# Kernel optimization log

Hardware: AMD Instinct MI355X
Metric: run time of the kernel (lower is better)

## Reference

```python
import jax, jax.numpy as jnp
import numpy as np

NUM_TAGS = 64
START_TAG = 62
STOP_TAG = 63
NEG = -10000.0
B, L = 512, 512


def setup_inputs() -> dict:
    key = jax.random.key(0)
    k1, k2, k3 = jax.random.split(key, 3)
    inputs = jax.random.normal(k1, (B, L, NUM_TAGS), dtype=jnp.float32)
    tags = jax.random.randint(k2, (B, L), 0, 62)  # real tags only (exclude sentinels)
    mask = jnp.ones((B, L), dtype=jnp.int32)
    transitions = jax.random.normal(k3, (NUM_TAGS, NUM_TAGS), dtype=jnp.float32)
    # match torch __init__: transitions[start_tag, :] = -10000; transitions[:, stop_tag] = -10000
    transitions = transitions.at[START_TAG, :].set(NEG).at[:, STOP_TAG].set(NEG)
    return {"inputs": inputs, "tags": tags, "mask": mask, "transitions": transitions}


def crf_loss(inputs, transitions, tags, mask):
    # inputs: [B, L, T] emissions; transitions[next, prev]; tags/mask: [B, L]
    Bb, Ll, T = inputs.shape
    maskf = mask.astype(inputs.dtype)

    # ---- denominator: forward algorithm (log-sum-exp recurrence over time) ----
    init_alphas = jnp.full((Bb, T), NEG, dtype=inputs.dtype).at[:, START_TAG].set(0.0)

    def step(forward_var, xs):
        emit, m = xs  # emit: [B, T], m: [B]
        # scores[b, next, prev] = fv[b, prev] + (transitions[next, prev] + emit[b, next]) * m[b]
        scores = forward_var[:, None, :] + (transitions[None, :, :] + emit[:, :, None]) * m[:, None, None]
        return jax.nn.logsumexp(scores, axis=-1), None

    forward_var, _ = jax.lax.scan(step, init_alphas, (jnp.swapaxes(inputs, 0, 1), maskf.T))
    terminal = forward_var + transitions[STOP_TAG][None, :]
    log_denominator = jax.nn.logsumexp(terminal, axis=-1)  # [B]

    # ---- numerator: score of the gold tag sequence (fully vectorized over time) ----
    score = transitions[tags[:, 0], START_TAG]  # [B]
    prev_t, next_t = tags[:, :-1], tags[:, 1:]
    trans_sc = transitions[next_t, prev_t]  # [B, L-1]
    emit_sc = jnp.take_along_axis(inputs[:, :-1, :], prev_t[:, :, None], axis=2)[..., 0]  # [B, L-1]
    score = score + jnp.sum(trans_sc * maskf[:, 1:] + emit_sc * maskf[:, :-1], axis=1)
    last_emit = jnp.take_along_axis(inputs[:, -1, :], tags[:, -1:], axis=1)[:, 0]
    score = score + transitions[STOP_TAG, tags[:, -1]] + last_emit * maskf[:, -1]

    return jnp.sum(score - log_denominator)


def reference(inputs, tags, mask, transitions):
    return crf_loss(inputs, transitions, tags, mask)
```

## Files before the change

### kernel.cpp

```cpp
#include <hip/hip_runtime.h>

namespace {

typedef float v2f __attribute__((ext_vector_type(2)));

constexpr int NTAGS = 64;
constexpr int START_T = 62;
constexpr int STOP_T = 63;
constexpr int Bc = 512;
constexpr int Lc = 512;

template <int CTRL>
__device__ __forceinline__ float dpp_add(float x) {
  return x + __int_as_float(__builtin_amdgcn_update_dpp(
                 0, __float_as_int(x), CTRL, 0xf, 0xf, true));
}

__device__ __forceinline__ float wave_max(float v) {
#pragma unroll
  for (int off = 32; off >= 1; off >>= 1)
    v = fmaxf(v, __shfl_xor(v, off, 64));
  return v;
}

__device__ __forceinline__ float wave_sum(float v) {
#pragma unroll
  for (int off = 32; off >= 1; off >>= 1)
    v += __shfl_xor(v, off, 64);
  return v;
}

__global__ __launch_bounds__(64, 1) void crf_scan(
    const float* __restrict__ inputs,
    const int* __restrict__ tags,
    const int* __restrict__ mask,
    const float* __restrict__ trans,
    float* __restrict__ partial) {
  __shared__ float4 vb4[16];
  float* vb1 = reinterpret_cast<float*>(vb4);

  const int b = blockIdx.x;
  const int lane = threadIdx.x;
  const int lr = lane >> 2;
  const int c = lane & 3;

#define DECLE(k) v2f E##k##_0, E##k##_1, E##k##_2, E##k##_3, \
                     E##k##_4, E##k##_5, E##k##_6, E##k##_7;
  DECLE(0) DECLE(1) DECLE(2) DECLE(3)
#define LOADE(k)                                                       \
  {                                                                    \
    const float* tp = trans + (lr + 16 * k) * NTAGS + 4 * c;           \
    E##k##_0 = (v2f){__expf(tp[0]),  __expf(tp[16])};                  \
    E##k##_1 = (v2f){__expf(tp[32]), __expf(tp[48])};                  \
    E##k##_2 = (v2f){__expf(tp[1]),  __expf(tp[17])};                  \
    E##k##_3 = (v2f){__expf(tp[33]), __expf(tp[49])};                  \
    E##k##_4 = (v2f){__expf(tp[2]),  __expf(tp[18])};                  \
    E##k##_5 = (v2f){__expf(tp[34]), __expf(tp[50])};                  \
    E##k##_6 = (v2f){__expf(tp[3]),  __expf(tp[19])};                  \
    E##k##_7 = (v2f){__expf(tp[35]), __expf(tp[51])};                  \
  }
  LOADE(0) LOADE(1) LOADE(2) LOADE(3)

  const float* emit_base = inputs + (size_t)b * Lc * NTAGS;
  const int* mask_b = mask + b * Lc;
  const int* tags_b = tags + b * Lc;

  int Msum = 0;
  vb1[lane] = (lane == 59) ? 1.0f : 0.0f;
  __builtin_amdgcn_wave_barrier();

#define ROWF(k)                                                        \
    v2f a##k##0 = E##k##_0 * (v2f){u0.x, u0.y};                        \
    v2f a##k##1 = E##k##_1 * (v2f){u0.z, u0.w};                        \
    a##k##0 += E##k##_2 * (v2f){u1.x, u1.y};                           \
    a##k##1 += E##k##_3 * (v2f){u1.z, u1.w};                           \
    a##k##0 += E##k##_4 * (v2f){u2.x, u2.y};                           \
    a##k##1 += E##k##_5 * (v2f){u2.z, u2.w};                           \
    a##k##0 += E##k##_6 * (v2f){u3.x, u3.y};                           \
    a##k##1 += E##k##_7 * (v2f){u3.z, u3.w};

#define STEP(W0, W1, W2, W3, MIDX)                                     \
  {                                                                    \
    float4 u0 = vb4[4 * c + 0], u1 = vb4[4 * c + 1];                   \
    float4 u2 = vb4[4 * c + 2], u3 = vb4[4 * c + 3];                   \
        \
    const int sb = __builtin_amdgcn_readlane(__float_as_int(u0.x), 0); \
    const unsigned e0 = ((unsigned)sb >> 23) & 0xffu;                  \
    const int d = (e0 == 0u) ? 0 : (int)e0 - 127;                      \
    Msum += d;                                                         \
    const float rs = __uint_as_float((unsigned)(127 - d) << 23);       \
    const int mv = __builtin_amdgcn_readlane(mrow, (MIDX));            \
    float s0, s1, s2, s3;                                              \
    if (mv) {                                                          \
      ROWF(0) ROWF(1) ROWF(2) ROWF(3)                                  \
      v2f t0 = a00 + a01, t1 = a10 + a11;                              \
      v2f t2 = a20 + a21, t3 = a30 + a31;                              \
      s0 = t0.x + t0.y; s1 = t1.x + t1.y;                              \
      s2 = t2.x + t2.y; s3 = t3.x + t3.y;                              \
      s0 = dpp_add<0xB1>(s0); s1 = dpp_add<0xB1>(s1);                  \
      s2 = dpp_add<0xB1>(s2); s3 = dpp_add<0xB1>(s3);                  \
      s0 = dpp_add<0x4E>(s0); s1 = dpp_add<0x4E>(s1);                  \
      s2 = dpp_add<0x4E>(s2); s3 = dpp_add<0x4E>(s3);                  \
      s0 *= (W0) * rs; s1 *= (W1) * rs;                                \
      s2 *= (W2) * rs; s3 *= (W3) * rs;                                \
    } else {                                                           \
      v2f q0 = ((v2f){u0.x, u0.y} + (v2f){u0.z, u0.w}) +               \
               ((v2f){u1.x, u1.y} + (v2f){u1.z, u1.w});                \
      v2f q1 = ((v2f){u2.x, u2.y} + (v2f){u2.z, u2.w}) +               \
               ((v2f){u3.x, u3.y} + (v2f){u3.z, u3.w});                \
      v2f q = q0 + q1;                                                 \
      float ss = q.x + q.y;                                            \
      ss = dpp_add<0xB1>(ss); ss = dpp_add<0x4E>(ss);                  \
      ss *= rs;                                                        \
      s0 = s1 = s2 = s3 = ss;                                          \
    }                                                                  \
    __builtin_amdgcn_wave_barrier();                                   \
    if ((lane & 3) == 0) vb4[lr] = make_float4(s0, s1, s2, s3);        \
    __builtin_amdgcn_wave_barrier();                                   \
  }

  float wA[4][4], wB[4][4];
#define PRE(Wb, ST)                                                    \
  {                                                                    \
    int s_ = (ST); s_ = s_ > (Lc - 4) ? (Lc - 4) : s_;                 \
    _Pragma("unroll") for (int q = 0; q < 4; ++q) {                    \
      const float* pp = emit_base + (size_t)(s_ + q) * NTAGS + lr;     \
      Wb[q][0] = __expf(pp[0]);                                        \
      Wb[q][1] = __expf(pp[16]);                                       \
      Wb[q][2] = __expf(pp[32]);                                       \
      Wb[q][3] = __expf(pp[48]);                                       \
    }                                                                  \
  }

  PRE(wA, 0)
  int mrow = mask_b[lane];

  for (int chunk = 0; chunk < 8; ++chunk) {
    const int cbase = chunk * 64;
    int mrow_nxt = mask_b[(chunk < 7 ? cbase + 64 : cbase) + lane];
    for (int gp = 0; gp < 8; ++gp) {
      const int base = cbase + gp * 8;
      const int mb = gp * 8;
      PRE(wB, base + 4)
      STEP(wA[0][0], wA[0][1], wA[0][2], wA[0][3], mb + 0)
      STEP(wA[1][0], wA[1][1], wA[1][2], wA[1][3], mb + 1)
      STEP(wA[2][0], wA[2][1], wA[2][2], wA[2][3], mb + 2)
      STEP(wA[3][0], wA[3][1], wA[3][2], wA[3][3], mb + 3)
      PRE(wA, base + 8)
      STEP(wB[0][0], wB[0][1], wB[0][2], wB[0][3], mb + 4)
      STEP(wB[1][0], wB[1][1], wB[1][2], wB[1][3], mb + 5)
      STEP(wB[2][0], wB[2][1], wB[2][2], wB[2][3], mb + 6)
      STEP(wB[3][0], wB[3][1], wB[3][2], wB[3][3], mb + 7)
    }
    mrow = mrow_nxt;
  }

  const float mf = (float)Msum;
  const float C = fmaf(mf, -2.1219444e-4f, mf * 0.693359375f);

  const int sig = ((lane & 15) << 2) | (lane >> 4);
  float alphav = __logf(vb1[sig]) + C;
  float term = alphav + trans[STOP_T * NTAGS + lane];
  float mx = wave_max(term);
  float sden = wave_sum(__expf(term - mx));
  float logden = mx + __logf(sden);

  float sc = 0.0f;
  for (int l = lane; l < Lc; l += 64) {
    int tl = tags_b[l];
    float mfl = (float)mask_b[l];
    if (l < Lc - 1) {
      int tn = tags_b[l + 1];
      float mfn = (float)mask_b[l + 1];
      sc += trans[tn * NTAGS + tl] * mfn +
            emit_base[(size_t)l * NTAGS + tl] * mfl;
    } else {
      sc += trans[STOP_T * NTAGS + tl] +
            emit_base[(size_t)l * NTAGS + tl] * mfl;
    }
  }
  if (lane == 0) sc += trans[tags_b[0] * NTAGS + START_T];
  float score = wave_sum(sc);

  if (lane == 0) partial[b] = score - logden;
}

__global__ void crf_reduce(const float* __restrict__ partial,
                           float* __restrict__ out) {
  const int lane = threadIdx.x;
  float s = 0.0f;
  for (int i = lane; i < Bc; i += 64) s += partial[i];
  s = wave_sum(s);
  if (lane == 0) out[0] = s;
}

}

extern "C" void kernel_launch(void* const* d_in, const int* in_sizes, int n_in,
                              void* d_out, int out_size, void* d_ws,
                              size_t ws_size, hipStream_t stream) {
  const float* inputs = (const float*)d_in[0];
  const int* tags = (const int*)d_in[1];
  const int* mask = (const int*)d_in[2];
  const float* trans = (const float*)d_in[3];
  float* out = (float*)d_out;
  float* partial = (float*)d_ws;

  crf_scan<<<Bc, 64, 0, stream>>>(inputs, tags, mask, trans, partial);
  crf_reduce<<<1, 64, 0, stream>>>(partial, out);
}
```

Baseline: 157.9 us.

## Interleave four batch chains per wave and split numerator into separate kernel

Each wave now runs the forward recurrence for four sequences at once, interleaving their independent steps to hide LDS and DPP latency in the serial chain. The numerator score moves into its own kernel, and the reduce combines the two. Each step also loads its next state vector right after the LDS write, and every lane writes one element instead of quad-leader float4 stores. In exchange there are only 128 blocks on a 256-CU part, so fewer CUs are busy, and register pressure rises from the four sets of prefetched emission weights.

```diff
diff --git a/kernel.cpp b/kernel.cpp
--- a/kernel.cpp
+++ b/kernel.cpp
@@ -9,6 +9,7 @@
 constexpr int STOP_T = 63;
 constexpr int Bc = 512;
 constexpr int Lc = 512;
+constexpr int NCH = 4;
 
 template <int CTRL>
 __device__ __forceinline__ float dpp_add(float x) {
@@ -32,17 +33,15 @@
 
 __global__ __launch_bounds__(64, 1) void crf_scan(
     const float* __restrict__ inputs,
-    const int* __restrict__ tags,
     const int* __restrict__ mask,
     const float* __restrict__ trans,
-    float* __restrict__ partial) {
-  __shared__ float4 vb4[16];
-  float* vb1 = reinterpret_cast<float*>(vb4);
-
-  const int b = blockIdx.x;
+    float* __restrict__ den) {
+  __shared__ float4 vb4[NCH][16];
+
   const int lane = threadIdx.x;
   const int lr = lane >> 2;
   const int c = lane & 3;
+  const int bbase = blockIdx.x * NCH;
 
 #define DECLE(k) v2f E##k##_0, E##k##_1, E##k##_2, E##k##_3, \
                      E##k##_4, E##k##_5, E##k##_6, E##k##_7;
@@ -61,109 +60,156 @@
   }
   LOADE(0) LOADE(1) LOADE(2) LOADE(3)
 
-  const float* emit_base = inputs + (size_t)b * Lc * NTAGS;
-  const int* mask_b = mask + b * Lc;
-  const int* tags_b = tags + b * Lc;
-
-  int Msum = 0;
-  vb1[lane] = (lane == 59) ? 1.0f : 0.0f;
+#define DECLC(i)                                                       \
+  float4 u0_##i, u1_##i, u2_##i, u3_##i;                               \
+  float wA_##i[4][4], wB_##i[4][4];                                    \
+  int Ms_##i = 0, mr_##i, mrn_##i;                                     \
+  const float* pe_##i = inputs + (size_t)(bbase + i) * Lc * NTAGS + lr;\
+  const int* mp_##i = mask + (size_t)(bbase + i) * Lc;
+  DECLC(0) DECLC(1) DECLC(2) DECLC(3)
+
+#pragma unroll
+  for (int i = 0; i < NCH; ++i)
+    ((float*)&vb4[i][0])[lane] = (lane == 59) ? 1.0f : 0.0f;
   __builtin_amdgcn_wave_barrier();
 
-#define ROWF(k)                                                        \
-    v2f a##k##0 = E##k##_0 * (v2f){u0.x, u0.y};                        \
-    v2f a##k##1 = E##k##_1 * (v2f){u0.z, u0.w};                        \
-    a##k##0 += E##k##_2 * (v2f){u1.x, u1.y};                           \
-    a##k##1 += E##k##_3 * (v2f){u1.z, u1.w};                           \
-    a##k##0 += E##k##_4 * (v2f){u2.x, u2.y};                           \
-    a##k##1 += E##k##_5 * (v2f){u2.z, u2.w};                           \
-    a##k##0 += E##k##_6 * (v2f){u3.x, u3.y};                           \
-    a##k##1 += E##k##_7 * (v2f){u3.z, u3.w};
-
-#define STEP(W0, W1, W2, W3, MIDX)                                     \
-  {                                                                    \
-    float4 u0 = vb4[4 * c + 0], u1 = vb4[4 * c + 1];                   \
-    float4 u2 = vb4[4 * c + 2], u3 = vb4[4 * c + 3];                   \
-        \
-    const int sb = __builtin_amdgcn_readlane(__float_as_int(u0.x), 0); \
+#define ULOAD(i)                                                       \
+  {                                                                    \
+    u0_##i = vb4[i][4 * c + 0];                                        \
+    u1_##i = vb4[i][4 * c + 1];                                        \
+    u2_##i = vb4[i][4 * c + 2];                                        \
+    u3_##i = vb4[i][4 * c + 3];                                        \
+  }
+  ULOAD(0) ULOAD(1) ULOAD(2) ULOAD(3)
+
+#define ROWF(k, i)                                                     \
+    v2f a##k##0 = E##k##_0 * (v2f){u0_##i.x, u0_##i.y};                \
+    v2f a##k##1 = E##k##_1 * (v2f){u0_##i.z, u0_##i.w};                \
+    a##k##0 += E##k##_2 * (v2f){u1_##i.x, u1_##i.y};                   \
+    a##k##1 += E##k##_3 * (v2f){u1_##i.z, u1_##i.w};                   \
+    a##k##0 += E##k##_4 * (v2f){u2_##i.x, u2_##i.y};                   \
+    a##k##1 += E##k##_5 * (v2f){u2_##i.z, u2_##i.w};                   \
+    a##k##0 += E##k##_6 * (v2f){u3_##i.x, u3_##i.y};                   \
+    a##k##1 += E##k##_7 * (v2f){u3_##i.z, u3_##i.w};
+
+#define STEP(i, W0, W1, W2, W3, MIDX)                                  \
+  {                                                                    \
+    const int sb =                                                     \
+        __builtin_amdgcn_readfirstlane(__float_as_int(u0_##i.x));      \
     const unsigned e0 = ((unsigned)sb >> 23) & 0xffu;                  \
     const int d = (e0 == 0u) ? 0 : (int)e0 - 127;                      \
-    Msum += d;                                                         \
+    Ms_##i += d;                                                       \
     const float rs = __uint_as_float((unsigned)(127 - d) << 23);       \
-    const int mv = __builtin_amdgcn_readlane(mrow, (MIDX));            \
+    const int mv = __builtin_amdgcn_readlane(mr_##i, (MIDX));          \
     float s0, s1, s2, s3;                                              \
-    if (mv) {                                                          \
-      ROWF(0) ROWF(1) ROWF(2) ROWF(3)                                  \
+    if (__builtin_expect(mv, 1)) {                                     \
+      ROWF(0, i) ROWF(1, i) ROWF(2, i) ROWF(3, i)                      \
       v2f t0 = a00 + a01, t1 = a10 + a11;                              \
       v2f t2 = a20 + a21, t3 = a30 + a31;                              \
-      s0 = t0.x + t0.y; s1 = t1.x + t1.y;                              \
-      s2 = t2.x + t2.y; s3 = t3.x + t3.y;                              \
-      s0 = dpp_add<0xB1>(s0); s1 = dpp_add<0xB1>(s1);                  \
-      s2 = dpp_add<0xB1>(s2); s3 = dpp_add<0xB1>(s3);                  \
-      s0 = dpp_add<0x4E>(s0); s1 = dpp_add<0x4E>(s1);                  \
-      s2 = dpp_add<0x4E>(s2); s3 = dpp_add<0x4E>(s3);                  \
-      s0 *= (W0) * rs; s1 *= (W1) * rs;                                \
-      s2 *= (W2) * rs; s3 *= (W3) * rs;                                \
+      float r0 = t0.x + t0.y, r1 = t1.x + t1.y;                        \
+      float r2 = t2.x + t2.y, r3 = t3.x + t3.y;                        \
+      r0 = dpp_add<0xB1>(r0); r1 = dpp_add<0xB1>(r1);                  \
+      r2 = dpp_add<0xB1>(r2); r3 = dpp_add<0xB1>(r3);                  \
+      r0 = dpp_add<0x4E>(r0); r1 = dpp_add<0x4E>(r1);                  \
+      r2 = dpp_add<0x4E>(r2); r3 = dpp_add<0x4E>(r3);                  \
+      s0 = r0 * ((W0) * rs); s1 = r1 * ((W1) * rs);                    \
+      s2 = r2 * ((W2) * rs); s3 = r3 * ((W3) * rs);                    \
     } else {                                                           \
-      v2f q0 = ((v2f){u0.x, u0.y} + (v2f){u0.z, u0.w}) +               \
-               ((v2f){u1.x, u1.y} + (v2f){u1.z, u1.w});                \
-      v2f q1 = ((v2f){u2.x, u2.y} + (v2f){u2.z, u2.w}) +               \
-               ((v2f){u3.x, u3.y} + (v2f){u3.z, u3.w});                \
-      v2f q = q0 + q1;                                                 \
-      float ss = q.x + q.y;                                            \
+      v2f q0 = ((v2f){u0_##i.x, u0_##i.y} + (v2f){u0_##i.z, u0_##i.w}) + \
+               ((v2f){u1_##i.x, u1_##i.y} + (v2f){u1_##i.z, u1_##i.w}); \
+      v2f q1 = ((v2f){u2_##i.x, u2_##i.y} + (v2f){u2_##i.z, u2_##i.w}) + \
+               ((v2f){u3_##i.x, u3_##i.y} + (v2f){u3_##i.z, u3_##i.w}); \
+      v2f qq = q0 + q1;                                                \
+      float ss = qq.x + qq.y;                                          \
       ss = dpp_add<0xB1>(ss); ss = dpp_add<0x4E>(ss);                  \
       ss *= rs;                                                        \
       s0 = s1 = s2 = s3 = ss;                                          \
     }                                                                  \
+        \
+    const float slo = (c & 1) ? s1 : s0;                               \
+    const float shi = (c & 1) ? s3 : s2;                               \
+    const float sw = (c & 2) ? shi : slo;                              \
     __builtin_amdgcn_wave_barrier();                                   \
-    if ((lane & 3) == 0) vb4[lr] = make_float4(s0, s1, s2, s3);        \
+    ((float*)&vb4[i][0])[lane] = sw;                                   \
     __builtin_amdgcn_wave_barrier();                                   \
-  }
-
-  float wA[4][4], wB[4][4];
-#define PRE(Wb, ST)                                                    \
+    ULOAD(i)                                                           \
+  }
+
+#define PRE(W, i, ST)                                                  \
   {                                                                    \
     int s_ = (ST); s_ = s_ > (Lc - 4) ? (Lc - 4) : s_;                 \
-    _Pragma("unroll") for (int q = 0; q < 4; ++q) {                    \
-      const float* pp = emit_base + (size_t)(s_ + q) * NTAGS + lr;     \
-      Wb[q][0] = __expf(pp[0]);                                        \
-      Wb[q][1] = __expf(pp[16]);                                       \
-      Wb[q][2] = __expf(pp[32]);                                       \
-      Wb[q][3] = __expf(pp[48]);                                       \
+    _Pragma("unroll") for (int q_ = 0; q_ < 4; ++q_) {                 \
+      const float* pp = pe_##i + (size_t)(s_ + q_) * NTAGS;            \
+      W[q_][0] = __expf(pp[0]);                                        \
+      W[q_][1] = __expf(pp[16]);                                       \
+      W[q_][2] = __expf(pp[32]);                                       \
+      W[q_][3] = __expf(pp[48]);                                       \
     }                                                                  \
   }
 
-  PRE(wA, 0)
-  int mrow = mask_b[lane];
+  PRE(wA_0, 0, 0) PRE(wA_1, 1, 0) PRE(wA_2, 2, 0) PRE(wA_3, 3, 0)
+  mr_0 = mp_0[lane]; mr_1 = mp_1[lane];
+  mr_2 = mp_2[lane]; mr_3 = mp_3[lane];
+
+#define S4(BANK, S, MIDX)                                              \
+  STEP(0, BANK##_0[S][0], BANK##_0[S][1], BANK##_0[S][2],              \
+       BANK##_0[S][3], MIDX)                                           \
+  STEP(1, BANK##_1[S][0], BANK##_1[S][1], BANK##_1[S][2],              \
+       BANK##_1[S][3], MIDX)                                           \
+  STEP(2, BANK##_2[S][0], BANK##_2[S][1], BANK##_2[S][2],              \
+       BANK##_2[S][3], MIDX)                                           \
+  STEP(3, BANK##_3[S][0], BANK##_3[S][1], BANK##_3[S][2],              \
+       BANK##_3[S][3], MIDX)
 
   for (int chunk = 0; chunk < 8; ++chunk) {
     const int cbase = chunk * 64;
-    int mrow_nxt = mask_b[(chunk < 7 ? cbase + 64 : cbase) + lane];
+    const int nb = (chunk < 7 ? cbase + 64 : cbase) + lane;
+    mrn_0 = mp_0[nb]; mrn_1 = mp_1[nb];
+    mrn_2 = mp_2[nb]; mrn_3 = mp_3[nb];
     for (int gp = 0; gp < 8; ++gp) {
       const int base = cbase + gp * 8;
       const int mb = gp * 8;
-      PRE(wB, base + 4)
-      STEP(wA[0][0], wA[0][1], wA[0][2], wA[0][3], mb + 0)
-      STEP(wA[1][0], wA[1][1], wA[1][2], wA[1][3], mb + 1)
-      STEP(wA[2][0], wA[2][1], wA[2][2], wA[2][3], mb + 2)
-      STEP(wA[3][0], wA[3][1], wA[3][2], wA[3][3], mb + 3)
-      PRE(wA, base + 8)
-      STEP(wB[0][0], wB[0][1], wB[0][2], wB[0][3], mb + 4)
-      STEP(wB[1][0], wB[1][1], wB[1][2], wB[1][3], mb + 5)
-      STEP(wB[2][0], wB[2][1], wB[2][2], wB[2][3], mb + 6)
-      STEP(wB[3][0], wB[3][1], wB[3][2], wB[3][3], mb + 7)
+      PRE(wB_0, 0, base + 4) PRE(wB_1, 1, base + 4)
+      PRE(wB_2, 2, base + 4) PRE(wB_3, 3, base + 4)
+      S4(wA, 0, mb + 0)
+      S4(wA, 1, mb + 1)
+      S4(wA, 2, mb + 2)
+      S4(wA, 3, mb + 3)
+      PRE(wA_0, 0, base + 8) PRE(wA_1, 1, base + 8)
+      PRE(wA_2, 2, base + 8) PRE(wA_3, 3, base + 8)
+      S4(wB, 0, mb + 4)
+      S4(wB, 1, mb + 5)
+      S4(wB, 2, mb + 6)
+      S4(wB, 3, mb + 7)
     }
-    mrow = mrow_nxt;
-  }
-
-  const float mf = (float)Msum;
-  const float C = fmaf(mf, -2.1219444e-4f, mf * 0.693359375f);
+    mr_0 = mrn_0; mr_1 = mrn_1; mr_2 = mrn_2; mr_3 = mrn_3;
+  }
 
   const int sig = ((lane & 15) << 2) | (lane >> 4);
-  float alphav = __logf(vb1[sig]) + C;
-  float term = alphav + trans[STOP_T * NTAGS + lane];
-  float mx = wave_max(term);
-  float sden = wave_sum(__expf(term - mx));
-  float logden = mx + __logf(sden);
+  const float* tstop = trans + STOP_T * NTAGS;
+#define EPI(i)                                                         \
+  {                                                                    \
+    const float mf_ = (float)Ms_##i;                                   \
+    const float C_ = fmaf(mf_, -2.1219444e-4f, mf_ * 0.693359375f);    \
+    float alphav = __logf(((const float*)&vb4[i][0])[sig]) + C_;       \
+    float term = alphav + tstop[lane];                                 \
+    float mx = wave_max(term);                                         \
+    float sden = wave_sum(__expf(term - mx));                          \
+    if (lane == 0) den[bbase + i] = mx + __logf(sden);                 \
+  }
+  EPI(0) EPI(1) EPI(2) EPI(3)
+}
+
+__global__ void crf_num(const float* __restrict__ inputs,
+                        const int* __restrict__ tags,
+                        const int* __restrict__ mask,
+                        const float* __restrict__ trans,
+                        float* __restrict__ num) {
+  const int b = blockIdx.x;
+  const int lane = threadIdx.x;
+  const float* emit_base = inputs + (size_t)b * Lc * NTAGS;
+  const int* tags_b = tags + b * Lc;
+  const int* mask_b = mask + b * Lc;
 
   float sc = 0.0f;
   for (int l = lane; l < Lc; l += 64) {
@@ -181,15 +227,15 @@
   }
   if (lane == 0) sc += trans[tags_b[0] * NTAGS + START_T];
   float score = wave_sum(sc);
-
-  if (lane == 0) partial[b] = score - logden;
-}
-
-__global__ void crf_reduce(const float* __restrict__ partial,
+  if (lane == 0) num[b] = score;
+}
+
+__global__ void crf_reduce(const float* __restrict__ num,
+                           const float* __restrict__ den,
                            float* __restrict__ out) {
   const int lane = threadIdx.x;
   float s = 0.0f;
-  for (int i = lane; i < Bc; i += 64) s += partial[i];
+  for (int i = lane; i < Bc; i += 64) s += num[i] - den[i];
   s = wave_sum(s);
   if (lane == 0) out[0] = s;
 }
@@ -204,8 +250,10 @@
   const int* mask = (const int*)d_in[2];
   const float* trans = (const float*)d_in[3];
   float* out = (float*)d_out;
-  float* partial = (float*)d_ws;
-
-  crf_scan<<<Bc, 64, 0, stream>>>(inputs, tags, mask, trans, partial);
-  crf_reduce<<<1, 64, 0, stream>>>(partial, out);
-}
+  float* num = (float*)d_ws;
+  float* den = num + Bc;
+
+  crf_scan<<<Bc / NCH, 64, 0, stream>>>(inputs, mask, trans, den);
+  crf_num<<<Bc, 64, 0, stream>>>(inputs, tags, mask, trans, num);
+  crf_reduce<<<1, 64, 0, stream>>>(num, den, out);
+}
```

New measurement: 478.5 us. +203.1%, slower.

## Split CRF forward recurrence into forward and backward halves meeting at midpoint

Applied to the files above, without the earlier changes.

The serial 512-step log-space recurrence is split into a forward pass over the first 256 steps and a backward pass over the last 256 steps, each run by its own workgroup (2*B blocks). The halves are joined by a dot product in a new join kernel, so the serial dependency chain per block is halved and twice as many waves are launched to fill the GPU. The numerator moves to its own kernel, and the scale exponent is now tracked via readfirstlane of the value being written instead of re-reading LDS. This adds two kernel launches and a workspace round trip, and it changes how rescaling and masked steps are handled in the backward direction.

```diff
diff --git a/kernel.cpp b/kernel.cpp
--- a/kernel.cpp
+++ b/kernel.cpp
@@ -9,18 +9,12 @@
 constexpr int STOP_T = 63;
 constexpr int Bc = 512;
 constexpr int Lc = 512;
+constexpr int HL = 256;
 
 template <int CTRL>
 __device__ __forceinline__ float dpp_add(float x) {
   return x + __int_as_float(__builtin_amdgcn_update_dpp(
                  0, __float_as_int(x), CTRL, 0xf, 0xf, true));
-}
-
-__device__ __forceinline__ float wave_max(float v) {
-#pragma unroll
-  for (int off = 32; off >= 1; off >>= 1)
-    v = fmaxf(v, __shfl_xor(v, off, 64));
-  return v;
 }
 
 __device__ __forceinline__ float wave_sum(float v) {
@@ -32,114 +26,164 @@
 
 __global__ __launch_bounds__(64, 1) void crf_scan(
     const float* __restrict__ inputs,
-    const int* __restrict__ tags,
     const int* __restrict__ mask,
     const float* __restrict__ trans,
-    float* __restrict__ partial) {
+    float* __restrict__ hv,
+    int* __restrict__ msum_out) {
   __shared__ float4 vb4[16];
   float* vb1 = reinterpret_cast<float*>(vb4);
 
-  const int b = blockIdx.x;
   const int lane = threadIdx.x;
   const int lr = lane >> 2;
   const int c = lane & 3;
+  const int bid = blockIdx.x;
+  const bool bwd = bid >= Bc;
+  const int b = bwd ? bid - Bc : bid;
+
+#define TE(ROW, COL) \
+  __expf(trans[bwd ? (COL) * NTAGS + (ROW) : (ROW) * NTAGS + (COL)])
 
 #define DECLE(k) v2f E##k##_0, E##k##_1, E##k##_2, E##k##_3, \
                      E##k##_4, E##k##_5, E##k##_6, E##k##_7;
   DECLE(0) DECLE(1) DECLE(2) DECLE(3)
 #define LOADE(k)                                                       \
   {                                                                    \
-    const float* tp = trans + (lr + 16 * k) * NTAGS + 4 * c;           \
-    E##k##_0 = (v2f){__expf(tp[0]),  __expf(tp[16])};                  \
-    E##k##_1 = (v2f){__expf(tp[32]), __expf(tp[48])};                  \
-    E##k##_2 = (v2f){__expf(tp[1]),  __expf(tp[17])};                  \
-    E##k##_3 = (v2f){__expf(tp[33]), __expf(tp[49])};                  \
-    E##k##_4 = (v2f){__expf(tp[2]),  __expf(tp[18])};                  \
-    E##k##_5 = (v2f){__expf(tp[34]), __expf(tp[50])};                  \
-    E##k##_6 = (v2f){__expf(tp[3]),  __expf(tp[19])};                  \
-    E##k##_7 = (v2f){__expf(tp[35]), __expf(tp[51])};                  \
+    const int row = lr + 16 * k;                                       \
+    const int c4 = 4 * c;                                              \
+    E##k##_0 = (v2f){TE(row, c4 + 0), TE(row, c4 + 16)};               \
+    E##k##_1 = (v2f){TE(row, c4 + 32), TE(row, c4 + 48)};              \
+    E##k##_2 = (v2f){TE(row, c4 + 1), TE(row, c4 + 17)};               \
+    E##k##_3 = (v2f){TE(row, c4 + 33), TE(row, c4 + 49)};              \
+    E##k##_4 = (v2f){TE(row, c4 + 2), TE(row, c4 + 18)};               \
+    E##k##_5 = (v2f){TE(row, c4 + 34), TE(row, c4 + 50)};              \
+    E##k##_6 = (v2f){TE(row, c4 + 3), TE(row, c4 + 19)};               \
+    E##k##_7 = (v2f){TE(row, c4 + 35), TE(row, c4 + 51)};              \
   }
   LOADE(0) LOADE(1) LOADE(2) LOADE(3)
 
   const float* emit_base = inputs + (size_t)b * Lc * NTAGS;
+  const float* pe = emit_base + lr;
   const int* mask_b = mask + b * Lc;
-  const int* tags_b = tags + b * Lc;
 
   int Msum = 0;
-  vb1[lane] = (lane == 59) ? 1.0f : 0.0f;
+  int rep;
+  {
+    const int j = lr + 16 * c;
+    float iv;
+    if (!bwd) {
+      iv = (j == START_T) ? 1.0f : 0.0f;
+    } else {
+      const float rr = __expf(trans[STOP_T * NTAGS + j]);
+      const float wl = (mask_b[Lc - 1] != 0)
+                           ? __expf(emit_base[(size_t)(Lc - 1) * NTAGS + j])
+                           : 1.0f;
+      iv = rr * wl;
+    }
+    vb1[lane] = iv;
+    rep = __builtin_amdgcn_readfirstlane(__float_as_int(iv));
+  }
   __builtin_amdgcn_wave_barrier();
 
-#define ROWF(k)                                                        \
-    v2f a##k##0 = E##k##_0 * (v2f){u0.x, u0.y};                        \
-    v2f a##k##1 = E##k##_1 * (v2f){u0.z, u0.w};                        \
-    a##k##0 += E##k##_2 * (v2f){u1.x, u1.y};                           \
-    a##k##1 += E##k##_3 * (v2f){u1.z, u1.w};                           \
-    a##k##0 += E##k##_4 * (v2f){u2.x, u2.y};                           \
-    a##k##1 += E##k##_5 * (v2f){u2.z, u2.w};                           \
-    a##k##0 += E##k##_6 * (v2f){u3.x, u3.y};                           \
+  float4 u0, u1, u2, u3;
+#define ULOAD               \
+  {                         \
+    u0 = vb4[4 * c + 0];    \
+    u1 = vb4[4 * c + 1];    \
+    u2 = vb4[4 * c + 2];    \
+    u3 = vb4[4 * c + 3];    \
+  }
+  ULOAD
+
+#define ROWF(k)                                        \
+    v2f a##k##0 = E##k##_0 * (v2f){u0.x, u0.y};        \
+    v2f a##k##1 = E##k##_1 * (v2f){u0.z, u0.w};        \
+    a##k##0 += E##k##_2 * (v2f){u1.x, u1.y};           \
+    a##k##1 += E##k##_3 * (v2f){u1.z, u1.w};           \
+    a##k##0 += E##k##_4 * (v2f){u2.x, u2.y};           \
+    a##k##1 += E##k##_5 * (v2f){u2.z, u2.w};           \
+    a##k##0 += E##k##_6 * (v2f){u3.x, u3.y};           \
     a##k##1 += E##k##_7 * (v2f){u3.z, u3.w};
 
 #define STEP(W0, W1, W2, W3, MIDX)                                     \
   {                                                                    \
-    float4 u0 = vb4[4 * c + 0], u1 = vb4[4 * c + 1];                   \
-    float4 u2 = vb4[4 * c + 2], u3 = vb4[4 * c + 3];                   \
-        \
-    const int sb = __builtin_amdgcn_readlane(__float_as_int(u0.x), 0); \
-    const unsigned e0 = ((unsigned)sb >> 23) & 0xffu;                  \
+    const unsigned e0 = ((unsigned)rep >> 23) & 0xffu;                 \
     const int d = (e0 == 0u) ? 0 : (int)e0 - 127;                      \
     Msum += d;                                                         \
     const float rs = __uint_as_float((unsigned)(127 - d) << 23);       \
     const int mv = __builtin_amdgcn_readlane(mrow, (MIDX));            \
     float s0, s1, s2, s3;                                              \
-    if (mv) {                                                          \
+    if (__builtin_expect(mv, 1)) {                                     \
       ROWF(0) ROWF(1) ROWF(2) ROWF(3)                                  \
       v2f t0 = a00 + a01, t1 = a10 + a11;                              \
       v2f t2 = a20 + a21, t3 = a30 + a31;                              \
-      s0 = t0.x + t0.y; s1 = t1.x + t1.y;                              \
-      s2 = t2.x + t2.y; s3 = t3.x + t3.y;                              \
-      s0 = dpp_add<0xB1>(s0); s1 = dpp_add<0xB1>(s1);                  \
-      s2 = dpp_add<0xB1>(s2); s3 = dpp_add<0xB1>(s3);                  \
-      s0 = dpp_add<0x4E>(s0); s1 = dpp_add<0x4E>(s1);                  \
-      s2 = dpp_add<0x4E>(s2); s3 = dpp_add<0x4E>(s3);                  \
-      s0 *= (W0) * rs; s1 *= (W1) * rs;                                \
-      s2 *= (W2) * rs; s3 *= (W3) * rs;                                \
+      float r0 = t0.x + t0.y, r1 = t1.x + t1.y;                        \
+      float r2 = t2.x + t2.y, r3 = t3.x + t3.y;                        \
+      r0 = dpp_add<0xB1>(r0); r1 = dpp_add<0xB1>(r1);                  \
+      r2 = dpp_add<0xB1>(r2); r3 = dpp_add<0xB1>(r3);                  \
+      r0 = dpp_add<0x4E>(r0); r1 = dpp_add<0x4E>(r1);                  \
+      r2 = dpp_add<0x4E>(r2); r3 = dpp_add<0x4E>(r3);                  \
+      s0 = r0 * ((W0) * rs); s1 = r1 * ((W1) * rs);                    \
+      s2 = r2 * ((W2) * rs); s3 = r3 * ((W3) * rs);                    \
     } else {                                                           \
       v2f q0 = ((v2f){u0.x, u0.y} + (v2f){u0.z, u0.w}) +               \
                ((v2f){u1.x, u1.y} + (v2f){u1.z, u1.w});                \
       v2f q1 = ((v2f){u2.x, u2.y} + (v2f){u2.z, u2.w}) +               \
                ((v2f){u3.x, u3.y} + (v2f){u3.z, u3.w});                \
-      v2f q = q0 + q1;                                                 \
-      float ss = q.x + q.y;                                            \
+      v2f qq = q0 + q1;                                                \
+      float ss = qq.x + qq.y;                                          \
       ss = dpp_add<0xB1>(ss); ss = dpp_add<0x4E>(ss);                  \
       ss *= rs;                                                        \
-      s0 = s1 = s2 = s3 = ss;                                          \
+      s0 = bwd ? ss * (W0) : ss; s1 = bwd ? ss * (W1) : ss;            \
+      s2 = bwd ? ss * (W2) : ss; s3 = bwd ? ss * (W3) : ss;            \
     }                                                                  \
+    const float slo = (c & 1) ? s1 : s0;                               \
+    const float shi = (c & 1) ? s3 : s2;                               \
+    const float sw = (c & 2) ? shi : slo;                              \
+    rep = __builtin_amdgcn_readfirstlane(__float_as_int(sw));          \
     __builtin_amdgcn_wave_barrier();                                   \
-    if ((lane & 3) == 0) vb4[lr] = make_float4(s0, s1, s2, s3);        \
+    vb1[lane] = sw;                                                    \
     __builtin_amdgcn_wave_barrier();                                   \
+    ULOAD                                                              \
   }
 
   float wA[4][4], wB[4][4];
-#define PRE(Wb, ST)                                                    \
+#define PRE(W, ST)                                                     \
   {                                                                    \
-    int s_ = (ST); s_ = s_ > (Lc - 4) ? (Lc - 4) : s_;                 \
-    _Pragma("unroll") for (int q = 0; q < 4; ++q) {                    \
-      const float* pp = emit_base + (size_t)(s_ + q) * NTAGS + lr;     \
-      Wb[q][0] = __expf(pp[0]);                                        \
-      Wb[q][1] = __expf(pp[16]);                                       \
-      Wb[q][2] = __expf(pp[32]);                                       \
-      Wb[q][3] = __expf(pp[48]);                                       \
+    _Pragma("unroll") for (int q_ = 0; q_ < 4; ++q_) {                 \
+      const int k_ = (ST) + q_;                                        \
+      if (!bwd) {                                                      \
+        const int kk = (k_ < HL) ? k_ : (HL - 1);                      \
+        const float* pp = pe + (size_t)kk * NTAGS;                     \
+        W[q_][0] = __expf(pp[0]);                                      \
+        W[q_][1] = __expf(pp[16]);                                     \
+        W[q_][2] = __expf(pp[32]);                                     \
+        W[q_][3] = __expf(pp[48]);                                     \
+      } else if (k_ >= HL - 1) {                                       \
+        W[q_][0] = W[q_][1] = W[q_][2] = W[q_][3] = 1.0f;              \
+      } else {                                                         \
+        const int e_ = (Lc - 2) - k_;                                  \
+        if (mask_b[e_] != 0) {                                         \
+          const float* pp = pe + (size_t)e_ * NTAGS;                   \
+          W[q_][0] = __expf(pp[0]);                                    \
+          W[q_][1] = __expf(pp[16]);                                   \
+          W[q_][2] = __expf(pp[32]);                                   \
+          W[q_][3] = __expf(pp[48]);                                   \
+        } else {                                                       \
+          W[q_][0] = W[q_][1] = W[q_][2] = W[q_][3] = 1.0f;            \
+        }                                                              \
+      }                                                                \
     }                                                                  \
   }
 
   PRE(wA, 0)
-  int mrow = mask_b[lane];
-
-  for (int chunk = 0; chunk < 8; ++chunk) {
-    const int cbase = chunk * 64;
-    int mrow_nxt = mask_b[(chunk < 7 ? cbase + 64 : cbase) + lane];
+  int mrow = mask_b[bwd ? (Lc - 1 - lane) : lane];
+
+  for (int cc = 0; cc < 4; ++cc) {
+    const int nc = (cc < 3) ? cc + 1 : cc;
+    const int mrow_nxt =
+        mask_b[bwd ? (Lc - 1 - nc * 64 - lane) : (nc * 64 + lane)];
     for (int gp = 0; gp < 8; ++gp) {
-      const int base = cbase + gp * 8;
+      const int base = cc * 64 + gp * 8;
       const int mb = gp * 8;
       PRE(wB, base + 4)
       STEP(wA[0][0], wA[0][1], wA[0][2], wA[0][3], mb + 0)
@@ -155,15 +199,20 @@
     mrow = mrow_nxt;
   }
 
-  const float mf = (float)Msum;
-  const float C = fmaf(mf, -2.1219444e-4f, mf * 0.693359375f);
-
-  const int sig = ((lane & 15) << 2) | (lane >> 4);
-  float alphav = __logf(vb1[sig]) + C;
-  float term = alphav + trans[STOP_T * NTAGS + lane];
-  float mx = wave_max(term);
-  float sden = wave_sum(__expf(term - mx));
-  float logden = mx + __logf(sden);
+  hv[(size_t)bid * NTAGS + lane] = vb1[lane];
+  if (lane == 0) msum_out[bid] = Msum;
+}
+
+__global__ void crf_num(const float* __restrict__ inputs,
+                        const int* __restrict__ tags,
+                        const int* __restrict__ mask,
+                        const float* __restrict__ trans,
+                        float* __restrict__ num) {
+  const int b = blockIdx.x;
+  const int lane = threadIdx.x;
+  const float* emit_base = inputs + (size_t)b * Lc * NTAGS;
+  const int* tags_b = tags + b * Lc;
+  const int* mask_b = mask + b * Lc;
 
   float sc = 0.0f;
   for (int l = lane; l < Lc; l += 64) {
@@ -181,8 +230,23 @@
   }
   if (lane == 0) sc += trans[tags_b[0] * NTAGS + START_T];
   float score = wave_sum(sc);
-
-  if (lane == 0) partial[b] = score - logden;
+  if (lane == 0) num[b] = score;
+}
+
+__global__ void crf_join(const float* __restrict__ hv,
+                         const int* __restrict__ msum,
+                         const float* __restrict__ num,
+                         float* __restrict__ partial) {
+  const int b = blockIdx.x;
+  const int lane = threadIdx.x;
+  const float prod = hv[(size_t)b * NTAGS + lane] *
+                     hv[(size_t)(b + Bc) * NTAGS + lane];
+  const float sden = wave_sum(prod);
+  if (lane == 0) {
+    const float mf = (float)(msum[b] + msum[b + Bc]);
+    const float C = fmaf(mf, -2.1219444e-4f, mf * 0.693359375f);
+    partial[b] = num[b] - (__logf(sden) + C);
+  }
 }
 
 __global__ void crf_reduce(const float* __restrict__ partial,
@@ -204,8 +268,14 @@
   const int* mask = (const int*)d_in[2];
   const float* trans = (const float*)d_in[3];
   float* out = (float*)d_out;
-  float* partial = (float*)d_ws;
-
-  crf_scan<<<Bc, 64, 0, stream>>>(inputs, tags, mask, trans, partial);
+
+  float* num = (float*)d_ws;
+  float* partial = num + Bc;
+  float* hv = partial + Bc;
+  int* msum = (int*)(hv + 2 * Bc * NTAGS);
+
+  crf_scan<<<2 * Bc, 64, 0, stream>>>(inputs, mask, trans, hv, msum);
+  crf_num<<<Bc, 64, 0, stream>>>(inputs, tags, mask, trans, num);
+  crf_join<<<Bc, 64, 0, stream>>>(hv, msum, num, partial);
   crf_reduce<<<1, 64, 0, stream>>>(partial, out);
 }
```

Result: slower. 164.0 us (+3.9%).
